# Kernel optimization log

Measured on AMD Instinct MI355X. Metric: run time of the kernel, lower is better.

Reference implementation:

```python
import jax, jax.numpy as jnp
import numpy as np

N_NODES = 100000
N_EDGES = 3200000
IN_CH = 54
HID = 32        # hidden_channels (concat of 4 heads x 8)
OUT = 64        # out_channels (mean over 4 heads)
HEADS = 4
N_GRAPHS = 512


def _segment_softmax(logits, seg, num_segments):
    # logits: [E, H], seg: [E] target-node index
    m = jax.ops.segment_max(logits, seg, num_segments=num_segments)
    m = jnp.where(jnp.isfinite(m), m, 0.0)
    e = jnp.exp(logits - m[seg])
    s = jax.ops.segment_sum(e, seg, num_segments=num_segments)
    return e / (s[seg] + 1e-16)


def _gatv2(x, src, dst, Wl, bl, Wr, br, att, bias, concat):
    # GATv2Conv (PyG): x_l=lin_l(x), x_r=lin_r(x);
    # e_ij = att . leaky_relu(x_l[j] + x_r[i]); alpha = softmax over incoming edges of i;
    # out_i = sum_j alpha_ij * x_l[j]
    N = x.shape[0]
    H, C = att.shape
    xl = (x @ Wl + bl).reshape(N, H, C)
    xr = (x @ Wr + br).reshape(N, H, C)
    e = jax.nn.leaky_relu(xl[src] + xr[dst], 0.2)       # [E, H, C]
    logits = jnp.einsum('ehc,hc->eh', e, att)            # [E, H]
    alpha = _segment_softmax(logits, dst, N)             # [E, H]
    out = jax.ops.segment_sum(xl[src] * alpha[:, :, None], dst, num_segments=N)  # [N,H,C]
    out = out.reshape(N, H * C) if concat else out.mean(axis=1)
    return out + bias


def setup_inputs() -> dict:
    key = jax.random.key(0)
    ks = jax.random.split(key, 16)
    x = jax.random.normal(ks[0], (N_NODES, IN_CH), dtype=jnp.float32)
    edge_index = jax.random.randint(ks[1], (2, N_EDGES), 0, N_NODES, dtype=jnp.int64 if jax.config.jax_enable_x64 else jnp.int32)
    batch_index = jnp.sort(jax.random.randint(ks[2], (N_NODES,), 0, N_GRAPHS))
    C1 = HID // HEADS  # 8
    s1 = 1.0 / np.sqrt(IN_CH)
    s2 = 1.0 / np.sqrt(HID)
    inp = {
        'x': x, 'edge_index': edge_index, 'batch_index': batch_index,
        # layer 1: GATv2Conv(54 -> 8, heads=4, concat=True)
        'Wl1': jax.random.normal(ks[3], (IN_CH, HEADS * C1)) * s1,
        'bl1': jnp.zeros((HEADS * C1,), jnp.float32),
        'Wr1': jax.random.normal(ks[4], (IN_CH, HEADS * C1)) * s1,
        'br1': jnp.zeros((HEADS * C1,), jnp.float32),
        'att1': jax.random.normal(ks[5], (HEADS, C1)) * (1.0 / np.sqrt(C1)),
        'b1': jnp.zeros((HEADS * C1,), jnp.float32),
        # layer 2: GATv2Conv(32 -> 64, heads=4, concat=False)
        'Wl2': jax.random.normal(ks[6], (HID, HEADS * OUT)) * s2,
        'bl2': jnp.zeros((HEADS * OUT,), jnp.float32),
        'Wr2': jax.random.normal(ks[7], (HID, HEADS * OUT)) * s2,
        'br2': jnp.zeros((HEADS * OUT,), jnp.float32),
        'att2': jax.random.normal(ks[8], (HEADS, OUT)) * (1.0 / np.sqrt(OUT)),
        'b2': jnp.zeros((OUT,), jnp.float32),
    }
    return inp


def reference(x, edge_index, batch_index, Wl1, bl1, Wr1, br1, att1, b1,
              Wl2, bl2, Wr2, br2, att2, b2):
    N = x.shape[0]
    # GATv2Conv adds self-loops by default
    loop = jnp.arange(N, dtype=edge_index.dtype)
    src = jnp.concatenate([edge_index[0], loop])
    dst = jnp.concatenate([edge_index[1], loop])
    h = _gatv2(x, src, dst, Wl1, bl1, Wr1, br1, att1, b1, concat=True)
    h = jax.nn.relu(h)  # BasicGNN inter-layer activation (default 'relu')
    h = _gatv2(h, src, dst, Wl2, bl2, Wr2, br2, att2, b2, concat=False)
    # Mish activation
    h = h * jnp.tanh(jax.nn.softplus(h))
    # global mean pool
    sums = jax.ops.segment_sum(h, batch_index, num_segments=N_GRAPHS)
    cnt = jax.ops.segment_sum(jnp.ones((N,), h.dtype), batch_index, num_segments=N_GRAPHS)
    return sums / jnp.maximum(cnt, 1.0)[:, None]
```

## Files before the change

### kernel.cpp

```cpp
#include <hip/hip_runtime.h>
#include <hip/hip_fp16.h>
#include <cmath>

#define NN 100000
#define NE 3200000
#define ET (NE + NN)
#define IN_CH 54
#define HID 32
#define OUTC 64
#define NG 512

__device__ __forceinline__ float lrelu(float v){ return fmaxf(v, 0.2f*v); }
__device__ __forceinline__ float mishf(float v){
    float sp = (v > 20.f) ? v : log1pf(__expf(v));
    return v * tanhf(sp);
}

__global__ void k_count(const int* __restrict__ ei, int* __restrict__ deg){
    int e = blockIdx.x*blockDim.x + threadIdx.x;
    if (e >= ET) return;
    int dst = (e < NE) ? ei[NE + e] : (e - NE);
    atomicAdd(&deg[dst], 1);
}

__global__ void k_scan_a(const int* __restrict__ deg, int* __restrict__ bsum){
    int i = blockIdx.x*256 + threadIdx.x;
    int v = (i < NN) ? deg[i] : 0;
    __shared__ int ws[4];
    #pragma unroll
    for (int o = 1; o < 64; o <<= 1) v += __shfl_xor(v, o);
    if ((threadIdx.x & 63) == 0) ws[threadIdx.x >> 6] = v;
    __syncthreads();
    if (threadIdx.x == 0) bsum[blockIdx.x] = ws[0] + ws[1] + ws[2] + ws[3];
}

__global__ void k_scan_b(int* __restrict__ bsum, int nb){
    __shared__ int sh[512];
    int t = threadIdx.x;
    int orig = (t < nb) ? bsum[t] : 0;
    sh[t] = orig;
    __syncthreads();
    for (int o = 1; o < 512; o <<= 1){
        int v = (t >= o) ? sh[t-o] : 0;
        __syncthreads();
        sh[t] += v;
        __syncthreads();
    }
    if (t < nb) bsum[t] = sh[t] - orig;
}

__global__ void k_scan_c(const int* __restrict__ deg, const int* __restrict__ boff,
                         int* __restrict__ rp, int* __restrict__ cur){
    int b = blockIdx.x, t = threadIdx.x;
    int i = b*256 + t;
    int v = (i < NN) ? deg[i] : 0;
    __shared__ int sh[256];
    sh[t] = v;
    __syncthreads();
    for (int o = 1; o < 256; o <<= 1){
        int u = (t >= o) ? sh[t-o] : 0;
        __syncthreads();
        sh[t] += u;
        __syncthreads();
    }
    int excl = sh[t] - v + boff[b];
    if (i < NN){ rp[i] = excl; cur[i] = excl; }
    if (i == NN-1) rp[NN] = excl + v;
}

__global__ void k_fill(const int* __restrict__ ei, int* __restrict__ cur, int* __restrict__ col){
    int e = blockIdx.x*blockDim.x + threadIdx.x;
    if (e >= ET) return;
    int src = (e < NE) ? ei[e]      : (e - NE);
    int dst = (e < NE) ? ei[NE + e] : (e - NE);
    int p = atomicAdd(&cur[dst], 1);
    col[p] = src;
}

__global__ void k_gemm1(const float* __restrict__ x,
                        const float* __restrict__ Wl, const float* __restrict__ bl,
                        const float* __restrict__ Wr, const float* __restrict__ br,
                        __half* __restrict__ xl1, __half* __restrict__ xr1){
    int node = (blockIdx.x*blockDim.x + threadIdx.x) >> 6;
    int lane = threadIdx.x & 63;
    if (node >= NN) return;
    int c = lane & 31;
    const float* W = (lane < 32) ? Wl : Wr;
    float acc = (lane < 32) ? bl[c] : br[c];
    const float* xrow = x + (size_t)node * IN_CH;
    #pragma unroll 6
    for (int k = 0; k < IN_CH; ++k)
        acc += xrow[k] * W[k*HID + c];
    __half h = __float2half_rn(acc);
    if (lane < 32) xl1[node*HID + c] = h;
    else           xr1[node*HID + c] = h;
}

__global__ void k_edge1(const __half* __restrict__ xl1, const __half* __restrict__ xr1,
                        const float* __restrict__ att, const float* __restrict__ b1,
                        const int* __restrict__ rp, const int* __restrict__ col,
                        float* __restrict__ hout){
    int node = (blockIdx.x*blockDim.x + threadIdx.x) >> 6;
    int lane = threadIdx.x & 63;
    if (node >= NN) return;
    int cl = lane & 15;
    int slot = lane >> 4;
    float2 xr = __half22float2(*(const __half2*)&xr1[node*HID + 2*cl]);
    float2 at = *(const float2*)&att[2*cl];
    float s = 0.f, acc0 = 0.f, acc1 = 0.f;
    int lo = rp[node], hi = rp[node+1];
    int deg = hi - lo;
    int cols = col[lo + min(lane, deg-1)];
    int niter = (deg + 3) >> 2;
    int nit3 = ((niter + 2)/3)*3;

    auto eload = [&](int i)->unsigned{
        int idx  = slot + 4*i;
        int idxc = min(idx, deg-1);
        int src  = __shfl(cols, min(idxc, 63));
        if (idxc > 63) src = col[lo + idxc];
        return *(const unsigned*)&xl1[src*HID + 2*cl];
    };
    auto eproc = [&](unsigned q, int i){
        bool valid = (slot + 4*i) < deg;
        float2 xlv = __half22float2(__builtin_bit_cast(__half2, q));
        float v0 = lrelu(xlv.x + xr.x), v1 = lrelu(xlv.y + xr.y);
        float p = v0*at.x + v1*at.y;
        p += __shfl_xor(p, 1);
        p += __shfl_xor(p, 2);
        float w = valid ? __expf(p) : 0.f;
        s    += w;
        acc0 += w * xlv.x;
        acc1 += w * xlv.y;
    };

    unsigned q0 = eload(0);
    unsigned q1 = eload(1);
    unsigned q2 = eload(2);
    for (int i = 3; i < nit3; i += 3){
        eproc(q0, i-3); q0 = eload(i);
        eproc(q1, i-2); q1 = eload(i+1);
        eproc(q2, i-1); q2 = eload(i+2);
    }
    eproc(q0, nit3-3); eproc(q1, nit3-2); eproc(q2, nit3-1);

    acc0 += __shfl_xor(acc0, 16); acc0 += __shfl_xor(acc0, 32);
    acc1 += __shfl_xor(acc1, 16); acc1 += __shfl_xor(acc1, 32);
    s    += __shfl_xor(s,    16); s    += __shfl_xor(s,    32);
    if (slot == 0){
        float inv = 1.f / (s + 1e-16f);
        float2 bb = *(const float2*)&b1[2*cl];
        float2 o;
        o.x = fmaxf(acc0*inv + bb.x, 0.f);
        o.y = fmaxf(acc1*inv + bb.y, 0.f);
        *(float2*)&hout[node*HID + 2*cl] = o;
    }
}

__global__ __launch_bounds__(256) void k_gemm2(const float* __restrict__ h,
                        const float* __restrict__ Wl, const float* __restrict__ bl,
                        __half* __restrict__ xl2){
    __shared__ float WS[HID*256];
    for (int i = threadIdx.x; i < HID*256; i += 256) WS[i] = Wl[i];
    __syncthreads();
    int lane = threadIdx.x & 63, wv = threadIdx.x >> 6;
    float4 b4 = *(const float4*)&bl[4*lane];
    int node0 = blockIdx.x * 32 + wv * 8;
    int nend = min(node0 + 8, NN);
    for (int n = node0; n < nend; ++n){
        const float* hr = h + n*HID;
        float4 a = {0.f,0.f,0.f,0.f};
        #pragma unroll 8
        for (int k = 0; k < HID; ++k){
            float hk = hr[k];
            float4 w = *(const float4*)&WS[k*256 + 4*lane];
            a.x += hk*w.x; a.y += hk*w.y; a.z += hk*w.z; a.w += hk*w.w;
        }
        ushort4 u;
        u.x = __half_as_ushort(__float2half_rn(a.x + b4.x));
        u.y = __half_as_ushort(__float2half_rn(a.y + b4.y));
        u.z = __half_as_ushort(__float2half_rn(a.z + b4.z));
        u.w = __half_as_ushort(__float2half_rn(a.w + b4.w));
        *(ushort4*)&xl2[(size_t)n*256 + 4*lane] = u;
    }
}

__global__ __launch_bounds__(256) void k_edge2(const __half* __restrict__ xl2,
                        const float* __restrict__ h,
                        const float* __restrict__ Wr, const float* __restrict__ br,
                        const float* __restrict__ att, const float* __restrict__ b2,
                        const int* __restrict__ rp, const int* __restrict__ col,
                        const int* __restrict__ batch,
                        float* __restrict__ pool, float* __restrict__ cnt){
    int node = (blockIdx.x*blockDim.x + threadIdx.x) >> 6;
    int lane = threadIdx.x & 63;
    if (node >= NN) return;

    int co = 4*lane;
    float4 xr4 = *(const float4*)&br[co];
    {
        const float* hr = h + node*HID;
        #pragma unroll 8
        for (int k = 0; k < HID; ++k){
            float hk = hr[k];
            float4 w = *(const float4*)&Wr[k*256 + co];
            xr4.x += hk*w.x; xr4.y += hk*w.y; xr4.z += hk*w.z; xr4.w += hk*w.w;
        }
    }
    float4 at4 = *(const float4*)&att[co];
    float s = 0.f;
    float4 acc = {0.f,0.f,0.f,0.f};
    int lo = rp[node], hi = rp[node+1];
    int deg  = hi - lo;
    int degc = min(deg, 64);
    int cols = col[lo + min(lane, deg-1)];
    int nbt = (degc + 3) >> 2;
    int nb3 = ((nbt + 2)/3)*3;

    uint2 A0,A1,A2,A3, B0,B1,B2,B3, C0,C1,C2,C3;

#define GLD(P0,P1,P2,P3, b_) do { \
        int i0_ = 4*(b_); \
        int s0_ = __shfl(cols, min(i0_  , degc-1)); \
        int s1_ = __shfl(cols, min(i0_+1, degc-1)); \
        int s2_ = __shfl(cols, min(i0_+2, degc-1)); \
        int s3_ = __shfl(cols, min(i0_+3, degc-1)); \
        P0 = *(const uint2*)(xl2 + s0_*256 + co); \
        P1 = *(const uint2*)(xl2 + s1_*256 + co); \
        P2 = *(const uint2*)(xl2 + s2_*256 + co); \
        P3 = *(const uint2*)(xl2 + s3_*256 + co); \
    } while(0)

#define PROC1(q, ei_) do { \
        float2 f01 = __half22float2(__builtin_bit_cast(__half2, q.x)); \
        float2 f23 = __half22float2(__builtin_bit_cast(__half2, q.y)); \
        float v0 = lrelu(f01.x + xr4.x), v1 = lrelu(f01.y + xr4.y); \
        float v2 = lrelu(f23.x + xr4.z), v3 = lrelu(f23.y + xr4.w); \
        float p = v0*at4.x + v1*at4.y + v2*at4.z + v3*at4.w; \
        p += __shfl_xor(p, 1); p += __shfl_xor(p, 2); \
        p += __shfl_xor(p, 4); p += __shfl_xor(p, 8); \
        float w = ((ei_) < degc) ? __expf(p) : 0.f; \
        s += w; \
        acc.x += w*f01.x; acc.y += w*f01.y; acc.z += w*f23.x; acc.w += w*f23.y; \
    } while(0)

#define PROC4(P0,P1,P2,P3, b_) do { \
        PROC1(P0, 4*(b_)); PROC1(P1, 4*(b_)+1); \
        PROC1(P2, 4*(b_)+2); PROC1(P3, 4*(b_)+3); } while(0)

    GLD(A0,A1,A2,A3, 0);
    GLD(B0,B1,B2,B3, 1);
    GLD(C0,C1,C2,C3, 2);
    for (int b = 3; b < nb3; b += 3){
        PROC4(A0,A1,A2,A3, b-3); GLD(A0,A1,A2,A3, b);
        PROC4(B0,B1,B2,B3, b-2); GLD(B0,B1,B2,B3, b+1);
        PROC4(C0,C1,C2,C3, b-1); GLD(C0,C1,C2,C3, b+2);
    }
    PROC4(A0,A1,A2,A3, nb3-3);
    PROC4(B0,B1,B2,B3, nb3-2);
    PROC4(C0,C1,C2,C3, nb3-1);

    for (int e = lo + 64; e < hi; ++e){
        int src = col[e];
        uint2 q = *(const uint2*)(xl2 + src*256 + co);
        PROC1(q, 0);
    }
#undef GLD
#undef PROC1
#undef PROC4

    float inv = 1.f / (s + 1e-16f);
    float4 t; t.x = acc.x*inv; t.y = acc.y*inv; t.z = acc.z*inv; t.w = acc.w*inv;
    t.x += __shfl_xor(t.x, 16); t.y += __shfl_xor(t.y, 16);
    t.z += __shfl_xor(t.z, 16); t.w += __shfl_xor(t.w, 16);
    t.x += __shfl_xor(t.x, 32); t.y += __shfl_xor(t.y, 32);
    t.z += __shfl_xor(t.z, 32); t.w += __shfl_xor(t.w, 32);
    if (lane < 16){
        int g = batch[node];
        float4 bb = *(const float4*)&b2[co];
        float o0 = 0.25f*t.x + bb.x;
        float o1 = 0.25f*t.y + bb.y;
        float o2 = 0.25f*t.z + bb.z;
        float o3 = 0.25f*t.w + bb.w;
        float* pg = pool + g*OUTC + co;
        atomicAdd(pg+0, mishf(o0));
        atomicAdd(pg+1, mishf(o1));
        atomicAdd(pg+2, mishf(o2));
        atomicAdd(pg+3, mishf(o3));
        if (lane == 0) atomicAdd(&cnt[g], 1.0f);
    }
}

__global__ void k_pool(const float* __restrict__ pool, const float* __restrict__ cnt,
                       float* __restrict__ out){
    int i = blockIdx.x*blockDim.x + threadIdx.x;
    if (i >= NG*OUTC) return;
    out[i] = pool[i] / fmaxf(cnt[i >> 6], 1.0f);
}

extern "C" void kernel_launch(void* const* d_in, const int* in_sizes, int n_in,
                              void* d_out, int out_size, void* d_ws, size_t ws_size,
                              hipStream_t stream){
    const float* x    = (const float*)d_in[0];
    const int*   ei   = (const int*)  d_in[1];
    const int*   batch= (const int*)  d_in[2];
    const float* Wl1  = (const float*)d_in[3];
    const float* bl1  = (const float*)d_in[4];
    const float* Wr1  = (const float*)d_in[5];
    const float* br1  = (const float*)d_in[6];
    const float* att1 = (const float*)d_in[7];
    const float* b1   = (const float*)d_in[8];
    const float* Wl2  = (const float*)d_in[9];
    const float* bl2  = (const float*)d_in[10];
    const float* Wr2  = (const float*)d_in[11];
    const float* br2  = (const float*)d_in[12];
    const float* att2 = (const float*)d_in[13];
    const float* b2   = (const float*)d_in[14];
    float* out = (float*)d_out;

    char* ws = (char*)d_ws;
    size_t off = 0;
    auto alloc = [&](size_t bytes)->char*{
        char* p = ws + off; off += (bytes + 255) & ~(size_t)255; return p;
    };
    __half* xl1  = (__half*)alloc((size_t)NN*HID*2);
    __half* xr1  = (__half*)alloc((size_t)NN*HID*2);
    float*  hbuf = (float*) alloc((size_t)NN*HID*4);
    __half* xl2  = (__half*)alloc((size_t)NN*256*2);
    int*    deg  = (int*)   alloc((size_t)NN*4);
    int*    rp   = (int*)   alloc((size_t)(NN+1)*4);
    int*    cur  = (int*)   alloc((size_t)NN*4);
    int*    col  = (int*)   alloc((size_t)ET*4);
    float*  pool = (float*) alloc((size_t)NG*OUTC*4);
    float*  cnt  = (float*) alloc((size_t)NG*4);
    int*    bsum = (int*)   alloc((size_t)512*4);

    const int NB = (NN + 255) / 256;

    hipMemsetAsync(deg,  0, (size_t)NN*4,      stream);
    hipMemsetAsync(pool, 0, (size_t)NG*OUTC*4, stream);
    hipMemsetAsync(cnt,  0, (size_t)NG*4,      stream);

    k_count <<<(ET+255)/256, 256, 0, stream>>>(ei, deg);
    k_scan_a<<<NB, 256, 0, stream>>>(deg, bsum);
    k_scan_b<<<1, 512, 0, stream>>>(bsum, NB);
    k_scan_c<<<NB, 256, 0, stream>>>(deg, bsum, rp, cur);
    k_fill  <<<(ET+255)/256, 256, 0, stream>>>(ei, cur, col);
    k_gemm1 <<<(NN+3)/4, 256, 0, stream>>>(x, Wl1, bl1, Wr1, br1, xl1, xr1);
    k_edge1 <<<(NN+3)/4, 256, 0, stream>>>(xl1, xr1, att1, b1, rp, col, hbuf);
    k_gemm2 <<<(NN+31)/32, 256, 0, stream>>>(hbuf, Wl2, bl2, xl2);
    k_edge2 <<<(NN+3)/4, 256, 0, stream>>>(xl2, hbuf, Wr2, br2, att2, b2, rp, col, batch, pool, cnt);
    k_pool  <<<(NG*OUTC+255)/256, 256, 0, stream>>>(pool, cnt, out);
}
```

Baseline: 1.210 ms.

## Process four edges per wavefront in layer-2 edge kernel with 16-channel lanes

Measured after the change: 1.943 ms. 1.61x slower.

```diff
diff --git a/kernel.cpp b/kernel.cpp
--- a/kernel.cpp
+++ b/kernel.cpp
@@ -195,10 +195,15 @@
     int node = (blockIdx.x*blockDim.x + threadIdx.x) >> 6;
     int lane = threadIdx.x & 63;
     if (node >= NN) return;
-
-    int co = 4*lane;
-    float4 xr4 = *(const float4*)&br[co];
+    int wv   = (threadIdx.x >> 6);
+    int l16  = lane & 15, g = lane >> 4;
+    int hh   = l16 & 3, cc = l16 >> 2;
+    int chb  = hh*64 + cc*16;
+
+    __shared__ float xrs[4][256];
     {
+        int co = 4*lane;
+        float4 xr4 = *(const float4*)&br[co];
         const float* hr = h + node*HID;
         #pragma unroll 8
         for (int k = 0; k < HID; ++k){
@@ -206,89 +211,131 @@
             float4 w = *(const float4*)&Wr[k*256 + co];
             xr4.x += hk*w.x; xr4.y += hk*w.y; xr4.z += hk*w.z; xr4.w += hk*w.w;
         }
-    }
-    float4 at4 = *(const float4*)&att[co];
+        *(float4*)&xrs[wv][co] = xr4;
+    }
+    __syncthreads();
+
+    float xr[16], at[16];
+    #pragma unroll
+    for (int i = 0; i < 16; i += 4){
+        *(float4*)&xr[i] = *(const float4*)&xrs[wv][chb + i];
+        *(float4*)&at[i] = *(const float4*)&att[chb + i];
+    }
+
+    float acc[16];
+    #pragma unroll
+    for (int i = 0; i < 16; ++i) acc[i] = 0.f;
     float s = 0.f;
-    float4 acc = {0.f,0.f,0.f,0.f};
+
     int lo = rp[node], hi = rp[node+1];
     int deg  = hi - lo;
     int degc = min(deg, 64);
     int cols = col[lo + min(lane, deg-1)];
-    int nbt = (degc + 3) >> 2;
-    int nb3 = ((nbt + 2)/3)*3;
-
-    uint2 A0,A1,A2,A3, B0,B1,B2,B3, C0,C1,C2,C3;
-
-#define GLD(P0,P1,P2,P3, b_) do { \
-        int i0_ = 4*(b_); \
-        int s0_ = __shfl(cols, min(i0_  , degc-1)); \
-        int s1_ = __shfl(cols, min(i0_+1, degc-1)); \
-        int s2_ = __shfl(cols, min(i0_+2, degc-1)); \
-        int s3_ = __shfl(cols, min(i0_+3, degc-1)); \
-        P0 = *(const uint2*)(xl2 + s0_*256 + co); \
-        P1 = *(const uint2*)(xl2 + s1_*256 + co); \
-        P2 = *(const uint2*)(xl2 + s2_*256 + co); \
-        P3 = *(const uint2*)(xl2 + s3_*256 + co); \
+    int nst  = (degc + 3) >> 2;
+    int nst3 = ((nst + 2)/3)*3;
+
+    uint4 A0,A1, B0,B1, C0,C1;
+
+#define LOADQ(QA,QB, s_) do { \
+        int eic_ = min(4*(s_) + g, degc-1); \
+        int src_ = __shfl(cols, eic_); \
+        const __half* rp_ = xl2 + (size_t)src_*256 + chb; \
+        QA = *(const uint4*)rp_; \
+        QB = *(const uint4*)(rp_ + 8); \
     } while(0)
 
-#define PROC1(q, ei_) do { \
-        float2 f01 = __half22float2(__builtin_bit_cast(__half2, q.x)); \
-        float2 f23 = __half22float2(__builtin_bit_cast(__half2, q.y)); \
-        float v0 = lrelu(f01.x + xr4.x), v1 = lrelu(f01.y + xr4.y); \
-        float v2 = lrelu(f23.x + xr4.z), v3 = lrelu(f23.y + xr4.w); \
-        float p = v0*at4.x + v1*at4.y + v2*at4.z + v3*at4.w; \
-        p += __shfl_xor(p, 1); p += __shfl_xor(p, 2); \
-        p += __shfl_xor(p, 4); p += __shfl_xor(p, 8); \
-        float w = ((ei_) < degc) ? __expf(p) : 0.f; \
-        s += w; \
-        acc.x += w*f01.x; acc.y += w*f01.y; acc.z += w*f23.x; acc.w += w*f23.y; \
+#define PROC(QA,QB, s_) do { \
+        bool valid_ = (4*(s_) + g) < degc; \
+        float xlf[16]; float2 f_; \
+        f_ = __half22float2(__builtin_bit_cast(__half2, QA.x)); xlf[0]=f_.x; xlf[1]=f_.y; \
+        f_ = __half22float2(__builtin_bit_cast(__half2, QA.y)); xlf[2]=f_.x; xlf[3]=f_.y; \
+        f_ = __half22float2(__builtin_bit_cast(__half2, QA.z)); xlf[4]=f_.x; xlf[5]=f_.y; \
+        f_ = __half22float2(__builtin_bit_cast(__half2, QA.w)); xlf[6]=f_.x; xlf[7]=f_.y; \
+        f_ = __half22float2(__builtin_bit_cast(__half2, QB.x)); xlf[8]=f_.x; xlf[9]=f_.y; \
+        f_ = __half22float2(__builtin_bit_cast(__half2, QB.y)); xlf[10]=f_.x; xlf[11]=f_.y; \
+        f_ = __half22float2(__builtin_bit_cast(__half2, QB.z)); xlf[12]=f_.x; xlf[13]=f_.y; \
+        f_ = __half22float2(__builtin_bit_cast(__half2, QB.w)); xlf[14]=f_.x; xlf[15]=f_.y; \
+        float p = 0.f; \
+        _Pragma("unroll") \
+        for (int i = 0; i < 16; ++i){ \
+            float t_ = xlf[i] + xr[i]; \
+            p += lrelu(t_) * at[i]; \
+        } \
+        p += __shfl_xor(p, 4); \
+        p += __shfl_xor(p, 8); \
+        float w_ = valid_ ? __expf(p) : 0.f; \
+        s += w_; \
+        _Pragma("unroll") \
+        for (int i = 0; i < 16; ++i) acc[i] += w_ * xlf[i]; \
     } while(0)
 
-#define PROC4(P0,P1,P2,P3, b_) do { \
-        PROC1(P0, 4*(b_)); PROC1(P1, 4*(b_)+1); \
-        PROC1(P2, 4*(b_)+2); PROC1(P3, 4*(b_)+3); } while(0)
-
-    GLD(A0,A1,A2,A3, 0);
-    GLD(B0,B1,B2,B3, 1);
-    GLD(C0,C1,C2,C3, 2);
-    for (int b = 3; b < nb3; b += 3){
-        PROC4(A0,A1,A2,A3, b-3); GLD(A0,A1,A2,A3, b);
-        PROC4(B0,B1,B2,B3, b-2); GLD(B0,B1,B2,B3, b+1);
-        PROC4(C0,C1,C2,C3, b-1); GLD(C0,C1,C2,C3, b+2);
-    }
-    PROC4(A0,A1,A2,A3, nb3-3);
-    PROC4(B0,B1,B2,B3, nb3-2);
-    PROC4(C0,C1,C2,C3, nb3-1);
-
-    for (int e = lo + 64; e < hi; ++e){
-        int src = col[e];
-        uint2 q = *(const uint2*)(xl2 + src*256 + co);
-        PROC1(q, 0);
-    }
-#undef GLD
-#undef PROC1
-#undef PROC4
-
+    LOADQ(A0,A1, 0);
+    LOADQ(B0,B1, 1);
+    LOADQ(C0,C1, 2);
+    for (int st = 3; st < nst3; st += 3){
+        PROC(A0,A1, st-3); LOADQ(A0,A1, st);
+        PROC(B0,B1, st-2); LOADQ(B0,B1, st+1);
+        PROC(C0,C1, st-1); LOADQ(C0,C1, st+2);
+    }
+    PROC(A0,A1, nst3-3);
+    PROC(B0,B1, nst3-2);
+    PROC(C0,C1, nst3-1);
+
+    for (int eb = 64; eb < deg; eb += 4){
+        int ei  = eb + g;
+        int eic = min(ei, deg-1);
+        int src = col[lo + eic];
+        const __half* rp_ = xl2 + (size_t)src*256 + chb;
+        uint4 qa = *(const uint4*)rp_;
+        uint4 qb = *(const uint4*)(rp_ + 8);
+        bool valid_ = ei < deg;
+        float xlf[16]; float2 f_;
+        f_ = __half22float2(__builtin_bit_cast(__half2, qa.x)); xlf[0]=f_.x; xlf[1]=f_.y;
+        f_ = __half22float2(__builtin_bit_cast(__half2, qa.y)); xlf[2]=f_.x; xlf[3]=f_.y;
+        f_ = __half22float2(__builtin_bit_cast(__half2, qa.z)); xlf[4]=f_.x; xlf[5]=f_.y;
+        f_ = __half22float2(__builtin_bit_cast(__half2, qa.w)); xlf[6]=f_.x; xlf[7]=f_.y;
+        f_ = __half22float2(__builtin_bit_cast(__half2, qb.x)); xlf[8]=f_.x; xlf[9]=f_.y;
+        f_ = __half22float2(__builtin_bit_cast(__half2, qb.y)); xlf[10]=f_.x; xlf[11]=f_.y;
+        f_ = __half22float2(__builtin_bit_cast(__half2, qb.z)); xlf[12]=f_.x; xlf[13]=f_.y;
+        f_ = __half22float2(__builtin_bit_cast(__half2, qb.w)); xlf[14]=f_.x; xlf[15]=f_.y;
+        float p = 0.f;
+        #pragma unroll
+        for (int i = 0; i < 16; ++i){ float t_ = xlf[i] + xr[i]; p += lrelu(t_) * at[i]; }
+        p += __shfl_xor(p, 4);
+        p += __shfl_xor(p, 8);
+        float w_ = valid_ ? __expf(p) : 0.f;
+        s += w_;
+        #pragma unroll
+        for (int i = 0; i < 16; ++i) acc[i] += w_ * xlf[i];
+    }
+#undef LOADQ
+#undef PROC
+
+    s += __shfl_xor(s, 16); s += __shfl_xor(s, 32);
     float inv = 1.f / (s + 1e-16f);
-    float4 t; t.x = acc.x*inv; t.y = acc.y*inv; t.z = acc.z*inv; t.w = acc.w*inv;
-    t.x += __shfl_xor(t.x, 16); t.y += __shfl_xor(t.y, 16);
-    t.z += __shfl_xor(t.z, 16); t.w += __shfl_xor(t.w, 16);
-    t.x += __shfl_xor(t.x, 32); t.y += __shfl_xor(t.y, 32);
-    t.z += __shfl_xor(t.z, 32); t.w += __shfl_xor(t.w, 32);
-    if (lane < 16){
-        int g = batch[node];
-        float4 bb = *(const float4*)&b2[co];
-        float o0 = 0.25f*t.x + bb.x;
-        float o1 = 0.25f*t.y + bb.y;
-        float o2 = 0.25f*t.z + bb.z;
-        float o3 = 0.25f*t.w + bb.w;
-        float* pg = pool + g*OUTC + co;
-        atomicAdd(pg+0, mishf(o0));
-        atomicAdd(pg+1, mishf(o1));
-        atomicAdd(pg+2, mishf(o2));
-        atomicAdd(pg+3, mishf(o3));
-        if (lane == 0) atomicAdd(&cnt[g], 1.0f);
-    }
+    #pragma unroll
+    for (int i = 0; i < 16; ++i){
+        float a = acc[i];
+        a += __shfl_xor(a, 16); a += __shfl_xor(a, 32);
+        acc[i] = a * inv;
+    }
+    #pragma unroll
+    for (int i = 0; i < 16; ++i){
+        float a = acc[i];
+        a += __shfl_xor(a, 1); a += __shfl_xor(a, 2);
+        acc[i] = a;
+    }
+    int grp = batch[node];
+    if (g == 0 && hh == 0){
+        float* pg = pool + grp*OUTC;
+        #pragma unroll
+        for (int i = 0; i < 16; ++i){
+            int j = cc*16 + i;
+            float o = 0.25f*acc[i] + b2[j];
+            atomicAdd(pg + j, mishf(o));
+        }
+    }
+    if (lane == 0) atomicAdd(&cnt[grp], 1.0f);
 }
 
 __global__ void k_pool(const float* __restrict__ pool, const float* __restrict__ cnt,
```

## Use nontemporal gathers and direct col loads in GATv2 edge kernels

Applied to the files above, without the earlier changes.

New measurement: 1.297 ms. 7.1% more time.

```diff
diff --git a/kernel.cpp b/kernel.cpp
--- a/kernel.cpp
+++ b/kernel.cpp
@@ -110,21 +110,19 @@
     float s = 0.f, acc0 = 0.f, acc1 = 0.f;
     int lo = rp[node], hi = rp[node+1];
     int deg = hi - lo;
-    int cols = col[lo + min(lane, deg-1)];
     int niter = (deg + 3) >> 2;
-    int nit3 = ((niter + 2)/3)*3;
+    int e0 = lo + slot;
 
     auto eload = [&](int i)->unsigned{
-        int idx  = slot + 4*i;
-        int idxc = min(idx, deg-1);
-        int src  = __shfl(cols, min(idxc, 63));
-        if (idxc > 63) src = col[lo + idxc];
-        return *(const unsigned*)&xl1[src*HID + 2*cl];
+        int e = e0 + 4*i;
+        int ec = min(e, hi-1);
+        return __builtin_nontemporal_load(
+            (const unsigned*)&xl1[col[ec]*HID + 2*cl]);
     };
-    auto eproc = [&](unsigned q, int i){
-        bool valid = (slot + 4*i) < deg;
+    auto eproc = [&](unsigned q, bool valid){
         float2 xlv = __half22float2(__builtin_bit_cast(__half2, q));
-        float v0 = lrelu(xlv.x + xr.x), v1 = lrelu(xlv.y + xr.y);
+        float t0 = xlv.x + xr.x, t1 = xlv.y + xr.y;
+        float v0 = lrelu(t0), v1 = lrelu(t1);
         float p = v0*at.x + v1*at.y;
         p += __shfl_xor(p, 1);
         p += __shfl_xor(p, 2);
@@ -134,15 +132,16 @@
         acc1 += w * xlv.y;
     };
 
-    unsigned q0 = eload(0);
-    unsigned q1 = eload(1);
-    unsigned q2 = eload(2);
-    for (int i = 3; i < nit3; i += 3){
-        eproc(q0, i-3); q0 = eload(i);
-        eproc(q1, i-2); q1 = eload(i+1);
-        eproc(q2, i-1); q2 = eload(i+2);
-    }
-    eproc(q0, nit3-3); eproc(q1, nit3-2); eproc(q2, nit3-1);
+    unsigned q0 = eload(0); bool v0 = (e0 < hi);
+    unsigned q1 = 0;        bool v1 = false;
+    if (niter > 1){ q1 = eload(1); v1 = (e0 + 4 < hi); }
+    for (int i = 2; i < niter; ++i){
+        unsigned q2 = eload(i); bool v2 = (e0 + 4*i < hi);
+        eproc(q0, v0);
+        q0 = q1; v0 = v1; q1 = q2; v1 = v2;
+    }
+    eproc(q0, v0);
+    if (niter > 1) eproc(q1, v1);
 
     acc0 += __shfl_xor(acc0, 16); acc0 += __shfl_xor(acc0, 32);
     acc1 += __shfl_xor(acc1, 16); acc1 += __shfl_xor(acc1, 32);
@@ -217,7 +216,7 @@
     int nbt = (degc + 3) >> 2;
     int nb3 = ((nbt + 2)/3)*3;
 
-    uint2 A0,A1,A2,A3, B0,B1,B2,B3, C0,C1,C2,C3;
+    unsigned long long A0,A1,A2,A3, B0,B1,B2,B3, C0,C1,C2,C3;
 
 #define GLD(P0,P1,P2,P3, b_) do { \
         int i0_ = 4*(b_); \
@@ -225,15 +224,15 @@
         int s1_ = __shfl(cols, min(i0_+1, degc-1)); \
         int s2_ = __shfl(cols, min(i0_+2, degc-1)); \
         int s3_ = __shfl(cols, min(i0_+3, degc-1)); \
-        P0 = *(const uint2*)(xl2 + s0_*256 + co); \
-        P1 = *(const uint2*)(xl2 + s1_*256 + co); \
-        P2 = *(const uint2*)(xl2 + s2_*256 + co); \
-        P3 = *(const uint2*)(xl2 + s3_*256 + co); \
+        P0 = __builtin_nontemporal_load((const unsigned long long*)(xl2 + s0_*256 + co)); \
+        P1 = __builtin_nontemporal_load((const unsigned long long*)(xl2 + s1_*256 + co)); \
+        P2 = __builtin_nontemporal_load((const unsigned long long*)(xl2 + s2_*256 + co)); \
+        P3 = __builtin_nontemporal_load((const unsigned long long*)(xl2 + s3_*256 + co)); \
     } while(0)
 
 #define PROC1(q, ei_) do { \
-        float2 f01 = __half22float2(__builtin_bit_cast(__half2, q.x)); \
-        float2 f23 = __half22float2(__builtin_bit_cast(__half2, q.y)); \
+        float2 f01 = __half22float2(__builtin_bit_cast(__half2, (unsigned)((q) & 0xffffffffu))); \
+        float2 f23 = __half22float2(__builtin_bit_cast(__half2, (unsigned)((q) >> 32))); \
         float v0 = lrelu(f01.x + xr4.x), v1 = lrelu(f01.y + xr4.y); \
         float v2 = lrelu(f23.x + xr4.z), v3 = lrelu(f23.y + xr4.w); \
         float p = v0*at4.x + v1*at4.y + v2*at4.z + v3*at4.w; \
@@ -262,7 +261,8 @@
 
     for (int e = lo + 64; e < hi; ++e){
         int src = col[e];
-        uint2 q = *(const uint2*)(xl2 + src*256 + co);
+        unsigned long long q = __builtin_nontemporal_load(
+            (const unsigned long long*)(xl2 + src*256 + co));
         PROC1(q, 0);
     }
 #undef GLD
```
